# Optimization experiments

Hardware: AMD Instinct MI355X
Metric: run time of the kernel (lower is better)

Reference implementation:

```python
import jax, jax.numpy as jnp
import numpy as np

L, E, H, FF = 6, 768, 4, 3072
D = E // H
SCALE = float(E) ** -0.5  # note: source scales by embedding_size**-0.5, not head_dim
EPS = 1e-5


def layernorm(x, scale, bias):
    mu = jnp.mean(x, axis=-1, keepdims=True)
    var = jnp.mean((x - mu) ** 2, axis=-1, keepdims=True)
    return (x - mu) * jax.lax.rsqrt(var + EPS) * scale + bias


def setup_inputs() -> dict:
    key = jax.random.key(0)
    ks = jax.random.split(key, 16)
    s = 0.02
    inp = {
        "hidden_states": jax.random.normal(ks[0], (8, 1024, E), dtype=jnp.float32),
        "ln1_scale": jnp.ones((L, E), jnp.float32),
        "ln1_bias": jnp.zeros((L, E), jnp.float32),
        "wq": jax.random.normal(ks[1], (L, E, E), jnp.float32) * s,
        "wk": jax.random.normal(ks[2], (L, E, E), jnp.float32) * s,
        "wv": jax.random.normal(ks[3], (L, E, E), jnp.float32) * s,
        "wo": jax.random.normal(ks[4], (L, E, E), jnp.float32) * s,
        "bo": jnp.zeros((L, E), jnp.float32),
        "ln2_scale": jnp.ones((L, E), jnp.float32),
        "ln2_bias": jnp.zeros((L, E), jnp.float32),
        "w1": jax.random.normal(ks[5], (L, FF, E), jnp.float32) * s,
        "b1": jnp.zeros((L, FF), jnp.float32),
        "w2": jax.random.normal(ks[6], (L, E, FF), jnp.float32) * s,
        "b2": jnp.zeros((L, E), jnp.float32),
    }
    return inp


def _encoder(x, ln1_scale, ln1_bias, wq, wk, wv, wo, bo, ln2_scale, ln2_bias, w1, b1, w2, b2):
    B, S, _ = x.shape
    for i in range(L):
        h = layernorm(x, ln1_scale[i], ln1_bias[i])
        # torch Linear: y = x @ W.T
        q = (h @ wq[i].T).reshape(B, H, S, D)  # non-standard head split (reshape, no transpose) per source
        k = (h @ wk[i].T).reshape(B, H, S, D)
        v = (h @ wv[i].T).reshape(B, H, S, D)
        scores = jnp.einsum("bhsd,bhtd->bhst", q, k) * SCALE  # full SxS materialized, as in source
        attn = jax.nn.softmax(scores, axis=-1)
        o = jnp.einsum("bhst,bhtd->bhsd", attn, v)
        o = o.transpose(0, 2, 1, 3).reshape(B, S, E)
        x = x + (o @ wo[i].T + bo[i])
        h = layernorm(x, ln2_scale[i], ln2_bias[i])
        h = jax.nn.gelu(h @ w1[i].T + b1[i], approximate=False)  # nn.GELU default = exact erf
        x = x + (h @ w2[i].T + b2[i])  # dropout is identity in eval
    return x


def reference(hidden_states, ln1_scale, ln1_bias, wq, wk, wv, wo, bo, ln2_scale, ln2_bias, w1, b1, w2, b2):
    return _encoder(hidden_states, ln1_scale, ln1_bias, wq, wk, wv, wo, bo, ln2_scale, ln2_bias, w1, b1, w2, b2)
```

## Files before the change

kernel.cpp:

```cpp
#include <hip/hip_runtime.h>
#include <math.h>

typedef __attribute__((ext_vector_type(8))) __bf16 bf16x8;
typedef __attribute__((ext_vector_type(4))) __bf16 bf16x4;
typedef __attribute__((ext_vector_type(2))) __bf16 bf16x2;
typedef __attribute__((ext_vector_type(4))) float f32x4;

#define MFMA_BF16 __builtin_amdgcn_mfma_f32_16x16x32_bf16

constexpr int LAY = 6, E = 768, HH = 4, DH = 192, FF = 3072, BB = 8, SS = 1024, MM = 8192;
constexpr float ATT_SCALE = 0.03608439182435161f;

__device__ __forceinline__ void gl2lds16(const void* g, void* l) {
    __builtin_amdgcn_global_load_lds(
        (const __attribute__((address_space(1))) void*)g,
        (__attribute__((address_space(3))) void*)l, 16, 0, 0);
}

struct Cast6 {
    const float* src[6];
    __bf16* dst[6];
    int cum4[7];
};

__global__ __launch_bounds__(256) void cast6_kernel(Cast6 c, int total4) {
    int stride = gridDim.x * 256;
    for (int i = blockIdx.x * 256 + threadIdx.x; i < total4; i += stride) {
        int rgn = 0;
#pragma unroll
        for (int k = 1; k < 6; ++k) rgn += (i >= c.cum4[k]) ? 1 : 0;
        int off = i - c.cum4[rgn];
        f32x4 v = ((const f32x4*)c.src[rgn])[off];
        bf16x4 o;
        o[0] = (__bf16)v[0]; o[1] = (__bf16)v[1]; o[2] = (__bf16)v[2]; o[3] = (__bf16)v[3];
        ((bf16x4*)c.dst[rgn])[off] = o;
    }
}

__global__ __launch_bounds__(256) void ln_kernel(const float* __restrict__ x,
                                                 const float* __restrict__ gamma,
                                                 const float* __restrict__ beta,
                                                 __bf16* __restrict__ out) {
    size_t row = blockIdx.x;
    const float* xr = x + row * E;
    int t = threadIdx.x;
    float v0 = xr[t], v1 = xr[t + 256], v2 = xr[t + 512];
    float s = v0 + v1 + v2;
    float q = v0 * v0 + v1 * v1 + v2 * v2;
#pragma unroll
    for (int m = 1; m < 64; m <<= 1) { s += __shfl_xor(s, m); q += __shfl_xor(q, m); }
    __shared__ float red[8];
    int w = t >> 6;
    if ((t & 63) == 0) { red[w] = s; red[4 + w] = q; }
    __syncthreads();
    s = red[0] + red[1] + red[2] + red[3];
    q = red[4] + red[5] + red[6] + red[7];
    float mu = s * (1.0f / E);
    float var = q * (1.0f / E) - mu * mu;
    float rs = rsqrtf(var + 1e-5f);
    __bf16* orow = out + row * E;
    orow[t]       = (__bf16)((v0 - mu) * rs * gamma[t]       + beta[t]);
    orow[t + 256] = (__bf16)((v1 - mu) * rs * gamma[t + 256] + beta[t + 256]);
    orow[t + 512] = (__bf16)((v2 - mu) * rs * gamma[t + 512] + beta[t + 512]);
}

template <int EPI, int SPLITK>
__global__ __launch_bounds__(256, 4) void gemm128(
    const __bf16* __restrict__ A,
    const __bf16* __restrict__ B0, const __bf16* __restrict__ B1, const __bf16* __restrict__ B2,
    void* __restrict__ O0, void* __restrict__ O1, void* __restrict__ O2,
    const float* __restrict__ bias, int M, int N, int K) {
    __shared__ __bf16 lds[2 * 8192];
    int z = blockIdx.z;
    const __bf16* Bw;
    void* Out;
    int ksp;
    if constexpr (SPLITK > 1) {
        Bw = B0; Out = O0; ksp = z;
    } else {
        Bw = (z == 0) ? B0 : (z == 1) ? B1 : B2;
        Out = (z == 0) ? O0 : (z == 1) ? O1 : O2;
        ksp = 0;
    }
    int Keff = K / SPLITK;
    int t = threadIdx.x;
    int w = t >> 6, lane = t & 63, b4 = lane >> 4, r = lane & 15;
    int gx = gridDim.x;
    int nwg = gx * gridDim.y;
    int bid = blockIdx.y * gx + blockIdx.x;
    int cpx = nwg >> 3;
    int swz = (bid & 7) * cpx + (bid >> 3);
    int bx = swz % gx, by = swz / gx;
    int mbase = by * 128, nbase = bx * 128;
    int wr = w >> 1, wc = w & 1;
    const f32x4 fz = {0.f, 0.f, 0.f, 0.f};
    f32x4 acc[4][4];
#pragma unroll
    for (int a1 = 0; a1 < 4; ++a1)
#pragma unroll
        for (int a2 = 0; a2 < 4; ++a2) acc[a1][a2] = fz;
    const __bf16* Ap = A + (size_t)mbase * K + ksp * Keff;
    const __bf16* Bp = Bw + (size_t)nbase * K + ksp * Keff;
    int nk = Keff >> 6;

    const __bf16* sA[4];
    const __bf16* sB[4];
#pragma unroll
    for (int i = 0; i < 4; ++i) {
        int c = i * 256 + t;
        int row = c >> 3;
        int col = ((c ^ row) & 7) * 8;
        sA[i] = Ap + (size_t)row * K + col;
        sB[i] = Bp + (size_t)row * K + col;
    }

    int ch0 = ((b4) ^ (r & 7)) * 8;
    int ch1 = ((4 + b4) ^ (r & 7)) * 8;
    int arow = (wr * 64 + r) * 64;
    int brow = 8192 + (wc * 64 + r) * 64;

    for (int kt = 0; kt < nk; ++kt) {
#pragma unroll
        for (int i = 0; i < 4; ++i) {
            gl2lds16(sA[i], (void*)(lds + i * 2048 + w * 512));
            gl2lds16(sB[i], (void*)(lds + 8192 + i * 2048 + w * 512));
            sA[i] += 64; sB[i] += 64;
        }
        __syncthreads();
#pragma unroll
        for (int ks = 0; ks < 2; ++ks) {
            int chk = ks ? ch1 : ch0;
            bf16x8 af[4], bfr[4];
#pragma unroll
            for (int mi = 0; mi < 4; ++mi)
                af[mi] = *(const bf16x8*)(lds + arow + mi * 1024 + chk);
#pragma unroll
            for (int ni = 0; ni < 4; ++ni)
                bfr[ni] = *(const bf16x8*)(lds + brow + ni * 1024 + chk);
#pragma unroll
            for (int mi = 0; mi < 4; ++mi)
#pragma unroll
                for (int ni = 0; ni < 4; ++ni)
                    acc[mi][ni] = MFMA_BF16(af[mi], bfr[ni], acc[mi][ni], 0, 0, 0);
        }
        __syncthreads();
    }

#pragma unroll
    for (int mi = 0; mi < 4; ++mi) {
#pragma unroll
        for (int ni = 0; ni < 4; ++ni) {
            int col = nbase + wc * 64 + ni * 16 + r;
#pragma unroll
            for (int j = 0; j < 4; ++j) {
                int rowi = mbase + wr * 64 + mi * 16 + b4 * 4 + j;
                float v = acc[mi][ni][j];
                if constexpr (EPI == 0) {
                    ((__bf16*)Out)[(size_t)rowi * N + col] = (__bf16)v;
                } else if constexpr (EPI == 1) {
                    v += bias[col];
                    float g = 0.5f * v * (1.0f + erff(v * 0.70710678118654752f));
                    ((__bf16*)Out)[(size_t)rowi * N + col] = (__bf16)g;
                } else {
                    float* X = (float*)Out;
                    float add = v + (ksp == 0 ? bias[col] : 0.0f);
                    atomicAdd(&X[(size_t)rowi * N + col], add);
                }
            }
        }
    }
}

__global__ __launch_bounds__(256) void vtrans_kernel(const __bf16* __restrict__ v,
                                                     __bf16* __restrict__ vt) {
    __shared__ __bf16 tile[64 * 72];
    int bh = blockIdx.y;
    int si = blockIdx.x / 3, di = blockIdx.x % 3;
    int t = threadIdx.x;
    const __bf16* src = v + (size_t)bh * (SS * DH) + (size_t)(si * 64) * DH + di * 64;
#pragma unroll
    for (int i = 0; i < 2; ++i) {
        int c = i * 256 + t;
        int sl = c >> 3, dc = c & 7;
        *(bf16x8*)(tile + sl * 72 + dc * 8) = *(const bf16x8*)(src + (size_t)sl * DH + dc * 8);
    }
    __syncthreads();
    __bf16* dst = vt + ((size_t)bh * DH + di * 64) * SS + si * 64;
#pragma unroll
    for (int i = 0; i < 2; ++i) {
        int c = i * 256 + t;
        int dl = c >> 3, sc = c & 7;
        bf16x8 o;
#pragma unroll
        for (int e = 0; e < 8; ++e) o[e] = tile[(sc * 8 + e) * 72 + dl];
        *(bf16x8*)(dst + (size_t)dl * SS + sc * 8) = o;
    }
}

__global__ __launch_bounds__(256) void attn_kernel(const __bf16* __restrict__ qp,
                                                   const __bf16* __restrict__ kp,
                                                   const __bf16* __restrict__ vtp,
                                                   __bf16* __restrict__ ao) {
    __shared__ __bf16 smK[64 * 192];
    __shared__ __bf16 smVt[192 * 64];
    __shared__ __bf16 smP[4 * 16 * 72];
    int qt = blockIdx.x, h = blockIdx.y, b = blockIdx.z;
    int t = threadIdx.x, w = t >> 6, lane = t & 63, b4 = lane >> 4, r = lane & 15;
    size_t base = (size_t)b * (SS * E) + (size_t)h * (SS * DH);
    const __bf16* Q = qp + base;
    const __bf16* Kg = kp + base;
    const __bf16* VtG = vtp + (size_t)(b * HH + h) * DH * SS;
    int q0 = qt * 64 + w * 16;
    bf16x8 qf[6];
#pragma unroll
    for (int ks = 0; ks < 6; ++ks)
        qf[ks] = *(const bf16x8*)(Q + (size_t)(q0 + r) * DH + ks * 32 + b4 * 8);
    const f32x4 fz = {0.f, 0.f, 0.f, 0.f};
    f32x4 oacc[12];
#pragma unroll
    for (int i = 0; i < 12; ++i) oacc[i] = fz;
    float m_r[4], l_r[4];
#pragma unroll
    for (int j = 0; j < 4; ++j) { m_r[j] = -1e30f; l_r[j] = 0.f; }
    __bf16* smPw = smP + w * (16 * 72);

    for (int kt = 0; kt < 16; ++kt) {
        const __bf16* Ks = Kg + (size_t)kt * 64 * DH;
#pragma unroll
        for (int i = 0; i < 6; ++i) {
            int c = i * 256 + t;
            int row = c / 24, cc = c - row * 24;
            int scc = (cc & 0x18) | ((cc ^ row) & 7);
            gl2lds16(Ks + (size_t)row * DH + scc * 8,
                     (void*)(smK + (i * 256 + w * 64) * 8));
        }
#pragma unroll
        for (int i = 0; i < 6; ++i) {
            int c = i * 256 + t;
            int row = c >> 3, cc = c & 7;
            int scc = cc ^ (row & 7);
            gl2lds16(VtG + (size_t)row * SS + kt * 64 + scc * 8,
                     (void*)(smVt + (i * 256 + w * 64) * 8));
        }
        __syncthreads();
        f32x4 sc[4];
#pragma unroll
        for (int nt = 0; nt < 4; ++nt) sc[nt] = fz;
#pragma unroll
        for (int ks = 0; ks < 6; ++ks) {
#pragma unroll
            for (int nt = 0; nt < 4; ++nt) {
                int cc = ks * 4 + b4;
                int ccs = (cc & 0x18) | ((cc ^ r) & 7);
                bf16x8 kf = *(const bf16x8*)(smK + (nt * 16 + r) * 192 + ccs * 8);
                sc[nt] = MFMA_BF16(qf[ks], kf, sc[nt], 0, 0, 0);
            }
        }
#pragma unroll
        for (int nt = 0; nt < 4; ++nt) sc[nt] *= ATT_SCALE;
        float alpha[4];
#pragma unroll
        for (int j = 0; j < 4; ++j) {
            float mx = fmaxf(fmaxf(sc[0][j], sc[1][j]), fmaxf(sc[2][j], sc[3][j]));
#pragma unroll
            for (int msk = 1; msk < 16; msk <<= 1) mx = fmaxf(mx, __shfl_xor(mx, msk));
            float mn = fmaxf(m_r[j], mx);
            alpha[j] = __expf(m_r[j] - mn);
            m_r[j] = mn;
            float p0 = __expf(sc[0][j] - mn);
            float p1 = __expf(sc[1][j] - mn);
            float p2 = __expf(sc[2][j] - mn);
            float p3 = __expf(sc[3][j] - mn);
            sc[0][j] = p0; sc[1][j] = p1; sc[2][j] = p2; sc[3][j] = p3;
            float ps = p0 + p1 + p2 + p3;
#pragma unroll
            for (int msk = 1; msk < 16; msk <<= 1) ps += __shfl_xor(ps, msk);
            l_r[j] = l_r[j] * alpha[j] + ps;
        }
        {
            f32x4 a4 = {alpha[0], alpha[1], alpha[2], alpha[3]};
#pragma unroll
            for (int i = 0; i < 12; ++i) oacc[i] *= a4;
        }
#pragma unroll
        for (int nt = 0; nt < 4; ++nt)
#pragma unroll
            for (int j = 0; j < 4; ++j)
                smPw[(b4 * 4 + j) * 72 + nt * 16 + r] = (__bf16)sc[nt][j];
        __asm__ volatile("s_waitcnt lgkmcnt(0)" ::: "memory");
#pragma unroll
        for (int kt2 = 0; kt2 < 2; ++kt2) {
            bf16x8 pa = *(const bf16x8*)(smPw + r * 72 + kt2 * 32 + b4 * 8);
#pragma unroll
            for (int nt = 0; nt < 12; ++nt) {
                int ccs = (kt2 * 4 + b4) ^ (r & 7);
                bf16x8 vf = *(const bf16x8*)(smVt + (nt * 16 + r) * 64 + ccs * 8);
                oacc[nt] = MFMA_BF16(pa, vf, oacc[nt], 0, 0, 0);
            }
        }
        __syncthreads();
    }
    float inv[4];
#pragma unroll
    for (int j = 0; j < 4; ++j) inv[j] = 1.0f / l_r[j];
    __bf16* obase = ao + (size_t)b * (SS * E);
#pragma unroll
    for (int nt = 0; nt < 12; ++nt)
#pragma unroll
        for (int j = 0; j < 4; ++j) {
            int srow = q0 + b4 * 4 + j;
            obase[(size_t)srow * E + h * DH + nt * 16 + r] = (__bf16)(oacc[nt][j] * inv[j]);
        }
}

extern "C" void kernel_launch(void* const* d_in, const int* in_sizes, int n_in,
                              void* d_out, int out_size, void* d_ws, size_t ws_size,
                              hipStream_t stream) {
    const float* hs   = (const float*)d_in[0];
    const float* ln1s = (const float*)d_in[1];
    const float* ln1b = (const float*)d_in[2];
    const float* wq   = (const float*)d_in[3];
    const float* wk   = (const float*)d_in[4];
    const float* wv   = (const float*)d_in[5];
    const float* wo   = (const float*)d_in[6];
    const float* bo   = (const float*)d_in[7];
    const float* ln2s = (const float*)d_in[8];
    const float* ln2b = (const float*)d_in[9];
    const float* w1   = (const float*)d_in[10];
    const float* b1   = (const float*)d_in[11];
    const float* w2   = (const float*)d_in[12];
    const float* b2   = (const float*)d_in[13];
    float* X = (float*)d_out;

    char* ws = (char*)d_ws;
    size_t off = 0;
    auto alloc = [&](size_t bytes) {
        char* p = ws + off;
        off += (bytes + 255) & ~(size_t)255;
        return p;
    };
    __bf16* wq_b = (__bf16*)alloc((size_t)E * E * 2);
    __bf16* wk_b = (__bf16*)alloc((size_t)E * E * 2);
    __bf16* wv_b = (__bf16*)alloc((size_t)E * E * 2);
    __bf16* wo_b = (__bf16*)alloc((size_t)E * E * 2);
    __bf16* w1_b = (__bf16*)alloc((size_t)FF * E * 2);
    __bf16* w2_b = (__bf16*)alloc((size_t)FF * E * 2);
    __bf16* h_b  = (__bf16*)alloc((size_t)MM * E * 2);
    char* U = alloc((size_t)MM * FF * 2);
    const size_t SLOT = (size_t)MM * E * 2;
    __bf16* q_b  = (__bf16*)U;
    __bf16* k_b  = (__bf16*)(U + SLOT);
    __bf16* v_b  = (__bf16*)(U + 2 * SLOT);
    __bf16* vt_b = (__bf16*)(U + 3 * SLOT);
    __bf16* a_b  = (__bf16*)(U + 2 * SLOT);
    __bf16* f_b  = (__bf16*)U;

    hipMemcpyAsync(d_out, hs, (size_t)MM * E * 4, hipMemcpyDeviceToDevice, stream);

    for (int i = 0; i < LAY; ++i) {
        Cast6 c;
        c.src[0] = wq + (size_t)i * E * E;  c.dst[0] = wq_b;
        c.src[1] = wk + (size_t)i * E * E;  c.dst[1] = wk_b;
        c.src[2] = wv + (size_t)i * E * E;  c.dst[2] = wv_b;
        c.src[3] = wo + (size_t)i * E * E;  c.dst[3] = wo_b;
        c.src[4] = w1 + (size_t)i * FF * E; c.dst[4] = w1_b;
        c.src[5] = w2 + (size_t)i * FF * E; c.dst[5] = w2_b;
        int n4[6] = {E * E / 4, E * E / 4, E * E / 4, E * E / 4, FF * E / 4, FF * E / 4};
        c.cum4[0] = 0;
        for (int k = 0; k < 6; ++k) c.cum4[k + 1] = c.cum4[k] + n4[k];
        int total4 = c.cum4[6];
        cast6_kernel<<<1024, 256, 0, stream>>>(c, total4);

        ln_kernel<<<MM, 256, 0, stream>>>(X, ln1s + (size_t)i * E, ln1b + (size_t)i * E, h_b);

        gemm128<0, 1><<<dim3(E / 128, MM / 128, 3), 256, 0, stream>>>(
            h_b, wq_b, wk_b, wv_b, q_b, k_b, v_b, nullptr, MM, E, E);

        vtrans_kernel<<<dim3(48, 32), 256, 0, stream>>>(v_b, vt_b);

        attn_kernel<<<dim3(SS / 64, HH, BB), 256, 0, stream>>>(q_b, k_b, vt_b, a_b);

        gemm128<2, 2><<<dim3(E / 128, MM / 128, 2), 256, 0, stream>>>(
            a_b, wo_b, wo_b, wo_b, X, X, X, bo + (size_t)i * E, MM, E, E);

        ln_kernel<<<MM, 256, 0, stream>>>(X, ln2s + (size_t)i * E, ln2b + (size_t)i * E, h_b);

        gemm128<1, 1><<<dim3(FF / 128, MM / 128, 1), 256, 0, stream>>>(
            h_b, w1_b, w1_b, w1_b, f_b, f_b, f_b, b1 + (size_t)i * FF, MM, FF, E);

        gemm128<2, 2><<<dim3(E / 128, MM / 128, 2), 256, 0, stream>>>(
            f_b, w2_b, w2_b, w2_b, X, X, X, b2 + (size_t)i * E, MM, E, FF);
    }
}
```

Measured before the change: 1.778 ms.

## Double-buffer GEMM K-tiles, approximate GELU with tanh form, raise split-K to three

The GEMM now uses a 32-wide K tile held in two LDS buffers, so the next tile's global-to-LDS load is issued while the current tile is computed. The swizzle is adjusted for the narrower rows, and the occupancy hint rises from 4 to 5. Split-K for the output and FFN-down projections goes from 2 to 3 for more parallelism, at the cost of more atomic adds. The exact erf GELU is replaced by a tanh-style approximation computed through exp, which no longer matches the reference's exact GELU and adds numerical error.

```diff
diff --git a/kernel.cpp b/kernel.cpp
--- a/kernel.cpp
+++ b/kernel.cpp
@@ -15,6 +15,11 @@
     __builtin_amdgcn_global_load_lds(
         (const __attribute__((address_space(1))) void*)g,
         (__attribute__((address_space(3))) void*)l, 16, 0, 0);
+}
+
+__device__ __forceinline__ float gelu_fast(float v) {
+    float y2 = 1.5957691216057308f * v * (1.0f + 0.044715f * v * v);
+    return v * (1.0f - 1.0f / (__expf(y2) + 1.0f));
 }
 
 struct Cast6 {
@@ -65,7 +70,7 @@
 }
 
 template <int EPI, int SPLITK>
-__global__ __launch_bounds__(256, 4) void gemm128(
+__global__ __launch_bounds__(256, 5) void gemm128(
     const __bf16* __restrict__ A,
     const __bf16* __restrict__ B0, const __bf16* __restrict__ B1, const __bf16* __restrict__ B2,
     void* __restrict__ O0, void* __restrict__ O1, void* __restrict__ O2,
@@ -101,48 +106,50 @@
         for (int a2 = 0; a2 < 4; ++a2) acc[a1][a2] = fz;
     const __bf16* Ap = A + (size_t)mbase * K + ksp * Keff;
     const __bf16* Bp = Bw + (size_t)nbase * K + ksp * Keff;
-    int nk = Keff >> 6;
-
-    const __bf16* sA[4];
-    const __bf16* sB[4];
-#pragma unroll
-    for (int i = 0; i < 4; ++i) {
+    int nk = Keff >> 5;
+
+    const __bf16* sA[2];
+    const __bf16* sB[2];
+#pragma unroll
+    for (int i = 0; i < 2; ++i) {
         int c = i * 256 + t;
-        int row = c >> 3;
-        int col = ((c ^ row) & 7) * 8;
+        int row = c >> 2;
+        int col = ((c ^ row ^ (row >> 2)) & 3) * 8;
         sA[i] = Ap + (size_t)row * K + col;
         sB[i] = Bp + (size_t)row * K + col;
     }
 
-    int ch0 = ((b4) ^ (r & 7)) * 8;
-    int ch1 = ((4 + b4) ^ (r & 7)) * 8;
-    int arow = (wr * 64 + r) * 64;
-    int brow = 8192 + (wc * 64 + r) * 64;
-
+    int chnk = (b4 ^ (r & 3) ^ ((r >> 2) & 3)) * 8;
+    int arow = (wr * 64 + r) * 32 + chnk;
+    int brow = 4096 + (wc * 64 + r) * 32 + chnk;
+
+    auto stage = [&](int bufsel) {
+        __bf16* dst = lds + bufsel * 8192;
+#pragma unroll
+        for (int i = 0; i < 2; ++i) {
+            gl2lds16(sA[i], (void*)(dst + i * 2048 + w * 512));
+            gl2lds16(sB[i], (void*)(dst + 4096 + i * 2048 + w * 512));
+            sA[i] += 32; sB[i] += 32;
+        }
+    };
+
+    stage(0);
+    __syncthreads();
     for (int kt = 0; kt < nk; ++kt) {
-#pragma unroll
-        for (int i = 0; i < 4; ++i) {
-            gl2lds16(sA[i], (void*)(lds + i * 2048 + w * 512));
-            gl2lds16(sB[i], (void*)(lds + 8192 + i * 2048 + w * 512));
-            sA[i] += 64; sB[i] += 64;
-        }
-        __syncthreads();
-#pragma unroll
-        for (int ks = 0; ks < 2; ++ks) {
-            int chk = ks ? ch1 : ch0;
-            bf16x8 af[4], bfr[4];
-#pragma unroll
-            for (int mi = 0; mi < 4; ++mi)
-                af[mi] = *(const bf16x8*)(lds + arow + mi * 1024 + chk);
+        if (kt + 1 < nk) stage((kt + 1) & 1);
+        const __bf16* sa = lds + (kt & 1) * 8192;
+        bf16x8 af[4], bfr[4];
+#pragma unroll
+        for (int mi = 0; mi < 4; ++mi)
+            af[mi] = *(const bf16x8*)(sa + arow + mi * 512);
+#pragma unroll
+        for (int ni = 0; ni < 4; ++ni)
+            bfr[ni] = *(const bf16x8*)(sa + brow + ni * 512);
+#pragma unroll
+        for (int mi = 0; mi < 4; ++mi)
 #pragma unroll
             for (int ni = 0; ni < 4; ++ni)
-                bfr[ni] = *(const bf16x8*)(lds + brow + ni * 1024 + chk);
-#pragma unroll
-            for (int mi = 0; mi < 4; ++mi)
-#pragma unroll
-                for (int ni = 0; ni < 4; ++ni)
-                    acc[mi][ni] = MFMA_BF16(af[mi], bfr[ni], acc[mi][ni], 0, 0, 0);
-        }
+                acc[mi][ni] = MFMA_BF16(af[mi], bfr[ni], acc[mi][ni], 0, 0, 0);
         __syncthreads();
     }
 
@@ -159,8 +166,7 @@
                     ((__bf16*)Out)[(size_t)rowi * N + col] = (__bf16)v;
                 } else if constexpr (EPI == 1) {
                     v += bias[col];
-                    float g = 0.5f * v * (1.0f + erff(v * 0.70710678118654752f));
-                    ((__bf16*)Out)[(size_t)rowi * N + col] = (__bf16)g;
+                    ((__bf16*)Out)[(size_t)rowi * N + col] = (__bf16)gelu_fast(v);
                 } else {
                     float* X = (float*)Out;
                     float add = v + (ksp == 0 ? bias[col] : 0.0f);
@@ -380,7 +386,7 @@
 
         attn_kernel<<<dim3(SS / 64, HH, BB), 256, 0, stream>>>(q_b, k_b, vt_b, a_b);
 
-        gemm128<2, 2><<<dim3(E / 128, MM / 128, 2), 256, 0, stream>>>(
+        gemm128<2, 3><<<dim3(E / 128, MM / 128, 3), 256, 0, stream>>>(
             a_b, wo_b, wo_b, wo_b, X, X, X, bo + (size_t)i * E, MM, E, E);
 
         ln_kernel<<<MM, 256, 0, stream>>>(X, ln2s + (size_t)i * E, ln2b + (size_t)i * E, h_b);
@@ -388,7 +394,7 @@
         gemm128<1, 1><<<dim3(FF / 128, MM / 128, 1), 256, 0, stream>>>(
             h_b, w1_b, w1_b, w1_b, f_b, f_b, f_b, b1 + (size_t)i * FF, MM, FF, E);
 
-        gemm128<2, 2><<<dim3(E / 128, MM / 128, 2), 256, 0, stream>>>(
+        gemm128<2, 3><<<dim3(E / 128, MM / 128, 3), 256, 0, stream>>>(
             f_b, w2_b, w2_b, w2_b, X, X, X, b2 + (size_t)i * E, MM, E, FF);
     }
 }
```

Result: slower. 2.604 ms (+46.5%).
